# Kernel tuning notes

Hardware: AMD Instinct MI355X
Metric: run time of the kernel (lower is better)

Reference implementation:

```python
import jax, jax.numpy as jnp
import numpy as np

H = 128  # GRU hidden size


def gru_cell(x_t, h, W_ih, W_hh, b_ih, b_hh):
    # Standard torch GRU cell math.
    gi = x_t @ W_ih.T + b_ih            # (bs, 3H)
    gh = h @ W_hh.T + b_hh              # (bs, 3H)
    i_r, i_z, i_n = jnp.split(gi, 3, axis=-1)
    h_r, h_z, h_n = jnp.split(gh, 3, axis=-1)
    r = jax.nn.sigmoid(i_r + h_r)
    z = jax.nn.sigmoid(i_z + h_z)
    n = jnp.tanh(i_n + r * h_n)
    return (1.0 - z) * n + z * h


def setup_inputs() -> dict:
    key = jax.random.key(0)
    ks = jax.random.split(key, 16)
    bs, seq, emb, nc = 64, 1024, 300, 23
    s = 0.05
    inp = {
        "x": jax.random.normal(ks[0], (bs, seq, emb), jnp.float32),
        "adj": jax.random.uniform(ks[1], (bs, seq, seq), jnp.float32),
        "mask": jax.random.uniform(ks[2], (bs, seq, 1), jnp.float32),
        # GRU forward direction params (torch layout: W_ih (3H, emb), W_hh (3H, H))
        "W_ih_f": jax.random.normal(ks[3], (3 * H, emb), jnp.float32) * s,
        "W_hh_f": jax.random.normal(ks[4], (3 * H, H), jnp.float32) * s,
        "b_ih_f": jax.random.normal(ks[5], (3 * H,), jnp.float32) * s,
        "b_hh_f": jax.random.normal(ks[6], (3 * H,), jnp.float32) * s,
        # GRU backward direction params
        "W_ih_b": jax.random.normal(ks[7], (3 * H, emb), jnp.float32) * s,
        "W_hh_b": jax.random.normal(ks[8], (3 * H, H), jnp.float32) * s,
        "b_ih_b": jax.random.normal(ks[9], (3 * H,), jnp.float32) * s,
        "b_hh_b": jax.random.normal(ks[10], (3 * H,), jnp.float32) * s,
        # MLP head: Linear(300+256,128) -> Linear(128,64) -> Linear(64,23)
        "W1": jax.random.normal(ks[11], (128, emb + 2 * H), jnp.float32) * s,
        "b1": jnp.zeros((128,), jnp.float32),
        "W2": jax.random.normal(ks[12], (64, 128), jnp.float32) * s,
        "b2": jnp.zeros((64,), jnp.float32),
        "W3": jax.random.normal(ks[13], (nc, 64), jnp.float32) * s,
        "b3": jnp.zeros((nc,), jnp.float32),
    }
    return inp


def reference(x, adj, mask, W_ih_f, W_hh_f, b_ih_f, b_hh_f,
              W_ih_b, W_hh_b, b_ih_b, b_hh_b, W1, b1, W2, b2, W3, b3):
    x = x * mask                                   # (bs, seq, emb)
    bs, seq, emb = x.shape

    # --- bidirectional GRU, last-step output ---
    # Forward direction output at t = seq-1 is the final hidden of a full scan.
    h0 = jnp.zeros((bs, H), x.dtype)
    def step(h, x_t):
        h_new = gru_cell(x_t, h, W_ih_f, W_hh_f, b_ih_f, b_hh_f)
        return h_new, None
    h_fwd, _ = jax.lax.scan(step, h0, jnp.swapaxes(x, 0, 1))  # (bs, H)
    # Backward direction output at t = seq-1 is exactly ONE cell step on x[:, -1]
    # starting from the zero initial state (it has only consumed the last token).
    h_bwd = gru_cell(x[:, -1, :], h0, W_ih_b, W_hh_b, b_ih_b, b_hh_b)
    h = jnp.concatenate([h_fwd, h_bwd], axis=1)    # (bs, 2H)

    # --- gfm: sum_{i,j} x_i * x_j per feature == (sum_i x_i)^2 ---
    # (original code materializes a (bs, seq*seq, emb) tensor; adj is dead code)
    s = jnp.sum(x, axis=1)                         # (bs, emb)
    gfm = s * s                                    # (bs, emb)

    # --- MLP head (dropout is identity at eval) ---
    z = jnp.concatenate([h, gfm], axis=1)          # (bs, 2H + emb)
    z = jax.nn.relu(z @ W1.T + b1)
    z = jax.nn.relu(z @ W2.T + b2)
    logit = z @ W3.T + b3                          # (bs, num_class)
    return logit
```

## Files before the change

kernel.cpp:

```cpp
#include <hip/hip_runtime.h>
#include <hip/hip_bf16.h>

#define HH   128
#define EMB  300
#define SEQ  1024
#define BS   64
#define NG   384
#define NCHUNK 8

typedef __attribute__((ext_vector_type(8))) short  bf16x8;
typedef __attribute__((ext_vector_type(4))) float  f32x4;
typedef _Float16 f16x2 __attribute__((ext_vector_type(2)));

__device__ __forceinline__ unsigned short f2bf(float f) {
    unsigned int u = __float_as_uint(f);
    unsigned int r = (u + 0x7fffu + ((u >> 16) & 1u)) >> 16;
    return (unsigned short)r;
}
__device__ __forceinline__ float bf2f(unsigned short u) {
    return __uint_as_float((unsigned int)u << 16);
}
__device__ __forceinline__ float fexp(float x) { return __builtin_amdgcn_exp2f(x * 1.44269504088896f); }
__device__ __forceinline__ float fsig(float x) { return __builtin_amdgcn_rcpf(1.f + fexp(-x)); }
__device__ __forceinline__ float ftanh(float x){ return __builtin_amdgcn_rcpf(1.f + fexp(-2.f*x)) * 2.f - 1.f; }

__device__ __forceinline__ float dpp_pair_add(float x) {
    int y = __builtin_amdgcn_mov_dpp(__float_as_int(x), 0xB1, 0xF, 0xF, true);
    return x + __int_as_float(y);
}

#define BAR_LDS() asm volatile("s_waitcnt lgkmcnt(0)\n\ts_barrier" ::: "memory")

__global__ __launch_bounds__(512) void gi_gemm(const float* __restrict__ X,
                                               const float* __restrict__ mask,
                                               const float* __restrict__ W,
                                               const float* __restrict__ bias,
                                               const float* __restrict__ bhh2,
                                               unsigned short* __restrict__ out) {
    __shared__ __align__(16) unsigned short As[128 * 32];
    __shared__ __align__(16) unsigned short Bs[384 * 32];
    const int m0   = blockIdx.x * 128;
    const int tid  = threadIdx.x;
    const int row  = tid >> 2;
    const int seg  = tid & 3;
    const int wave = tid >> 6;
    const int lane = tid & 63;
    const int wm   = wave >> 2;
    const int wn   = wave & 3;
    const int r16  = lane & 15, kg = lane >> 4;

    f32x4 acc[4][6];
    #pragma unroll
    for (int m = 0; m < 4; ++m)
        #pragma unroll
        for (int n = 0; n < 6; ++n) acc[m][n] = (f32x4){0.f,0.f,0.f,0.f};

    const float mrow = mask[m0 + row];

    for (int k0 = 0; k0 < 320; k0 += 32) {
        {
            const float* src = X + (size_t)(m0 + row) * EMB + k0 + seg * 8;
            unsigned short tmp[8];
            if (k0 + seg * 8 + 7 < EMB) {
                float4 v0 = ((const float4*)src)[0];
                float4 v1 = ((const float4*)src)[1];
                tmp[0]=f2bf(v0.x*mrow); tmp[1]=f2bf(v0.y*mrow);
                tmp[2]=f2bf(v0.z*mrow); tmp[3]=f2bf(v0.w*mrow);
                tmp[4]=f2bf(v1.x*mrow); tmp[5]=f2bf(v1.y*mrow);
                tmp[6]=f2bf(v1.z*mrow); tmp[7]=f2bf(v1.w*mrow);
            } else {
                #pragma unroll
                for (int i = 0; i < 8; ++i) {
                    int c = k0 + seg * 8 + i;
                    float v = (c < EMB) ? src[i] : 0.f;
                    tmp[i] = f2bf(v * mrow);
                }
            }
            *(uint4*)&As[row * 32 + seg * 8] = *(const uint4*)tmp;
        }
        #pragma unroll
        for (int r3 = 0; r3 < 3; ++r3) {
            const int rowb = row + r3 * 128;
            const float* src = W + (size_t)rowb * EMB + k0 + seg * 8;
            unsigned short tmp[8];
            if (k0 + seg * 8 + 7 < EMB) {
                float4 v0 = ((const float4*)src)[0];
                float4 v1 = ((const float4*)src)[1];
                tmp[0]=f2bf(v0.x); tmp[1]=f2bf(v0.y); tmp[2]=f2bf(v0.z); tmp[3]=f2bf(v0.w);
                tmp[4]=f2bf(v1.x); tmp[5]=f2bf(v1.y); tmp[6]=f2bf(v1.z); tmp[7]=f2bf(v1.w);
            } else {
                #pragma unroll
                for (int i = 0; i < 8; ++i) {
                    int c = k0 + seg * 8 + i;
                    float v = (c < EMB) ? src[i] : 0.f;
                    tmp[i] = f2bf(v);
                }
            }
            *(uint4*)&Bs[rowb * 32 + seg * 8] = *(const uint4*)tmp;
        }
        __syncthreads();

        bf16x8 a[4], bfr[6];
        #pragma unroll
        for (int m = 0; m < 4; ++m)
            a[m] = *(const bf16x8*)&As[(wm * 64 + m * 16 + r16) * 32 + kg * 8];
        #pragma unroll
        for (int n = 0; n < 6; ++n)
            bfr[n] = *(const bf16x8*)&Bs[(wn * 96 + n * 16 + r16) * 32 + kg * 8];
        #pragma unroll
        for (int m = 0; m < 4; ++m)
            #pragma unroll
            for (int n = 0; n < 6; ++n)
                acc[m][n] = __builtin_amdgcn_mfma_f32_16x16x32_bf16(a[m], bfr[n], acc[m][n], 0, 0, 0);
        __syncthreads();
    }

    #pragma unroll
    for (int m = 0; m < 4; ++m) {
        const int rowb = m0 + wm * 64 + m * 16 + kg * 4;
        #pragma unroll
        for (int n = 0; n < 6; ++n) {
            const int col = wn * 96 + n * 16 + r16;
            const float bj = bias[col] + (col < 2 * HH ? bhh2[col] : 0.f);
            #pragma unroll
            for (int q = 0; q < 4; ++q)
                out[(size_t)(rowb + q) * NG + col] = f2bf(acc[m][n][q] + bj);
        }
    }
}

__global__ __launch_bounds__(320) void col_sum(const float* __restrict__ X,
                                               const float* __restrict__ mask,
                                               float* __restrict__ spart) {
    const int b = blockIdx.x, c = blockIdx.y;
    const int e = threadIdx.x;
    if (e >= EMB) return;
    const int tchunk = SEQ / NCHUNK;
    float acc = 0.f;
    const float* xb = X + ((size_t)b * SEQ + (size_t)c * tchunk) * EMB;
    const float* mb = mask + (size_t)b * SEQ + (size_t)c * tchunk;
    for (int t = 0; t < tchunk; ++t)
        acc += xb[(size_t)t * EMB + e] * mb[t];
    spart[((size_t)b * NCHUNK + c) * EMB + e] = acc;
}

__global__ __launch_bounds__(256, 1) void gru_scan(const unsigned short* __restrict__ gi,
                                                   const float* __restrict__ Whh,
                                                   const float* __restrict__ bhh,
                                                   float* __restrict__ hout) {
    const int b    = blockIdx.x;
    const int tid  = threadIdx.x;
    const int j    = tid >> 1;
    const int half = tid & 1;
    __shared__ __align__(16) _Float16 hb[2][HH];

    f16x2 wr_[32], wz_[32], wn_[32];
    {
        const float2* r0 = (const float2*)(Whh + (size_t)j * HH            + half * 64);
        const float2* r1 = (const float2*)(Whh + (size_t)(j + HH) * HH     + half * 64);
        const float2* r2 = (const float2*)(Whh + (size_t)(j + 2 * HH) * HH + half * 64);
        #pragma unroll
        for (int i = 0; i < 32; ++i) {
            float2 a = r0[i], c = r1[i], d = r2[i];
            wr_[i] = (f16x2){(_Float16)a.x, (_Float16)a.y};
            wz_[i] = (f16x2){(_Float16)c.x, (_Float16)c.y};
            wn_[i] = (f16x2){(_Float16)d.x, (_Float16)d.y};
        }
    }
    const float bn_ = bhh[j + 2 * HH];

    float hreg = 0.f;
    if (tid < HH) hb[0][tid] = (_Float16)0.f;
    const unsigned short* gb = gi + (size_t)b * SEQ * NG;

    float gAr, gAz, gAn, gBr, gBz, gBn, gCr, gCz, gCn, gDr, gDz, gDn;
    {
        const unsigned short* g0 = gb;          gAr = bf2f(g0[j]); gAz = bf2f(g0[j+HH]); gAn = bf2f(g0[j+2*HH]);
        const unsigned short* g1 = gb + NG;     gBr = bf2f(g1[j]); gBz = bf2f(g1[j+HH]); gBn = bf2f(g1[j+2*HH]);
        const unsigned short* g2 = gb + 2 * NG; gCr = bf2f(g2[j]); gCz = bf2f(g2[j+HH]); gCn = bf2f(g2[j+2*HH]);
        const unsigned short* g3 = gb + 3 * NG; gDr = bf2f(g3[j]); gDz = bf2f(g3[j+HH]); gDn = bf2f(g3[j+2*HH]);
    }
    const unsigned short* pA = gb + 4 * NG;
    const unsigned short* pB = gb + 5 * NG;
    const unsigned short* pC = gb + 6 * NG;
    const unsigned short* pD = gb + 7 * NG;
    BAR_LDS();

#define GRU_BODY(P, GR, GZ, GN, PP)                                            \
    {                                                                          \
        float ar[2] = {0.f, 0.f}, az[2] = {0.f, 0.f}, an[2] = {0.f, 0.f};      \
        const uint4* hp = (const uint4*)&hb[P][half * 64];                     \
        _Pragma("unroll")                                                      \
        for (int i = 0; i < 8; ++i) {                                          \
            union { uint4 u; f16x2 h2[4]; } U;                                 \
            U.u = hp[i];                                                       \
            _Pragma("unroll")                                                  \
            for (int k = 0; k < 4; ++k) {                                      \
                ar[k&1] = __builtin_amdgcn_fdot2(wr_[i*4+k], U.h2[k], ar[k&1], false); \
                az[k&1] = __builtin_amdgcn_fdot2(wz_[i*4+k], U.h2[k], az[k&1], false); \
                an[k&1] = __builtin_amdgcn_fdot2(wn_[i*4+k], U.h2[k], an[k&1], false); \
            }                                                                  \
        }                                                                      \
        const float arf = dpp_pair_add(ar[0] + ar[1]);                         \
        const float azf = dpp_pair_add(az[0] + az[1]);                         \
        const float anf = dpp_pair_add(an[0] + an[1]);                         \
        const float r = fsig(GR + arf);                                        \
        const float z = fsig(GZ + azf);                                        \
        const float n = ftanh(GN + r * (anf + bn_));                           \
        hreg = n + z * (hreg - n);                                             \
        if (!half) hb[P ^ 1][j] = (_Float16)hreg;                              \
        GR = bf2f(PP[j]); GZ = bf2f(PP[j + HH]); GN = bf2f(PP[j + 2 * HH]);    \
        PP += 4 * NG;                                                          \
        BAR_LDS();                                                             \
    }

    for (int it = 0; it < SEQ / 4; ++it) {
        GRU_BODY(0, gAr, gAz, gAn, pA)
        GRU_BODY(1, gBr, gBz, gBn, pB)
        GRU_BODY(0, gCr, gCz, gCn, pC)
        GRU_BODY(1, gDr, gDz, gDn, pD)
    }
#undef GRU_BODY
    if (!half) hout[b * HH + j] = hreg;
}

__global__ __launch_bounds__(128) void mlp(const float* __restrict__ X,
                                           const float* __restrict__ mask,
                                           const float* __restrict__ WihB,
                                           const float* __restrict__ bihB,
                                           const float* __restrict__ bhhB,
                                           const float* __restrict__ hf,
                                           const float* __restrict__ spart,
                                           const float* __restrict__ W1, const float* __restrict__ b1,
                                           const float* __restrict__ W2, const float* __restrict__ b2,
                                           const float* __restrict__ W3, const float* __restrict__ b3,
                                           float* __restrict__ out) {
    const int b = blockIdx.x, j = threadIdx.x;
    __shared__ float xl[EMB];
    __shared__ float zin[2 * HH + EMB];
    __shared__ float l1[128];
    __shared__ float l2[64];

    const float* xr = X + ((size_t)b * SEQ + (SEQ - 1)) * EMB;
    const float  mv = mask[(size_t)b * SEQ + SEQ - 1];
    for (int e = j; e < EMB; e += 128) xl[e] = xr[e];
    zin[j] = hf[b * HH + j];
    for (int e = j; e < EMB; e += 128) {
        float v = 0.f;
        #pragma unroll
        for (int c = 0; c < NCHUNK; ++c)
            v += spart[((size_t)b * NCHUNK + c) * EMB + e];
        zin[2 * HH + e] = v * v;
    }
    __syncthreads();

    {
        const float* wR = WihB + (size_t)j * EMB;
        const float* wZ = WihB + (size_t)(j + HH) * EMB;
        const float* wN = WihB + (size_t)(j + 2 * HH) * EMB;
        float aR = 0.f, aZ = 0.f, aN = 0.f;
        for (int e = 0; e < EMB; ++e) {
            const float xv = xl[e];
            aR += xv * wR[e]; aZ += xv * wZ[e]; aN += xv * wN[e];
        }
        const float r = fsig(aR * mv + bihB[j] + bhhB[j]);
        const float z = fsig(aZ * mv + bihB[j + HH] + bhhB[j + HH]);
        const float n = ftanh(aN * mv + bihB[j + 2 * HH] + r * bhhB[j + 2 * HH]);
        zin[HH + j] = (1.f - z) * n;
    }
    __syncthreads();

    {
        float a = b1[j];
        const float* w = W1 + (size_t)j * (2 * HH + EMB);
        for (int i = 0; i < 2 * HH + EMB; ++i) a += zin[i] * w[i];
        l1[j] = fmaxf(a, 0.f);
    }
    __syncthreads();
    if (j < 64) {
        float a = b2[j];
        const float* w = W2 + (size_t)j * 128;
        for (int i = 0; i < 128; ++i) a += l1[i] * w[i];
        l2[j] = fmaxf(a, 0.f);
    }
    __syncthreads();
    if (j < 23) {
        float a = b3[j];
        const float* w = W3 + (size_t)j * 64;
        for (int i = 0; i < 64; ++i) a += l2[i] * w[i];
        out[b * 23 + j] = a;
    }
}

extern "C" void kernel_launch(void* const* d_in, const int* in_sizes, int n_in,
                              void* d_out, int out_size, void* d_ws, size_t ws_size,
                              hipStream_t stream) {
    const float* x     = (const float*)d_in[0];
    const float* mask  = (const float*)d_in[2];
    const float* Wih_f = (const float*)d_in[3];
    const float* Whh_f = (const float*)d_in[4];
    const float* bih_f = (const float*)d_in[5];
    const float* bhh_f = (const float*)d_in[6];
    const float* Wih_b = (const float*)d_in[7];
    const float* bih_b = (const float*)d_in[9];
    const float* bhh_b = (const float*)d_in[10];
    const float* W1 = (const float*)d_in[11];
    const float* b1 = (const float*)d_in[12];
    const float* W2 = (const float*)d_in[13];
    const float* b2 = (const float*)d_in[14];
    const float* W3 = (const float*)d_in[15];
    const float* b3 = (const float*)d_in[16];
    float* out = (float*)d_out;

    unsigned short* gi16 = (unsigned short*)d_ws;
    float* spart = (float*)(gi16 + (size_t)BS * SEQ * NG);
    float* hf    = spart + (size_t)BS * NCHUNK * EMB;

    gi_gemm<<<dim3(512), dim3(512), 0, stream>>>(x, mask, Wih_f, bih_f, bhh_f, gi16);
    col_sum<<<dim3(BS, NCHUNK), dim3(320), 0, stream>>>(x, mask, spart);
    gru_scan<<<dim3(BS), dim3(256), 0, stream>>>(gi16, Whh_f, bhh_f, hf);
    mlp<<<dim3(BS), dim3(128), 0, stream>>>(x, mask, Wih_b, bih_b, bhh_b, hf, spart,
                                            W1, b1, W2, b2, W3, b3, out);
}
```

Measured before the change: 579.0 us.

## Batch GRU recurrence across 16 sequences per block using f16 MFMA

The recurrent h@W_hh product moves from per-sequence fdot2 with one block per batch element to 16x16x32 f16 MFMA instructions, batching 16 sequences per block. That cuts the grid to 4 blocks, with weights held in registers as MFMA fragments and hidden state exchanged through a swizzled LDS buffer. The input-gate buffer also goes from bf16 to fp32, doubling its memory traffic but removing conversions and bf16 rounding error. The risk is that only 4 CUs are used for the sequential scan, and each step now loads more gi data per thread.

```diff
diff --git a/kernel.cpp b/kernel.cpp
--- a/kernel.cpp
+++ b/kernel.cpp
@@ -10,24 +10,16 @@
 
 typedef __attribute__((ext_vector_type(8))) short  bf16x8;
 typedef __attribute__((ext_vector_type(4))) float  f32x4;
-typedef _Float16 f16x2 __attribute__((ext_vector_type(2)));
+typedef _Float16 f16x8 __attribute__((ext_vector_type(8)));
 
 __device__ __forceinline__ unsigned short f2bf(float f) {
     unsigned int u = __float_as_uint(f);
     unsigned int r = (u + 0x7fffu + ((u >> 16) & 1u)) >> 16;
     return (unsigned short)r;
 }
-__device__ __forceinline__ float bf2f(unsigned short u) {
-    return __uint_as_float((unsigned int)u << 16);
-}
 __device__ __forceinline__ float fexp(float x) { return __builtin_amdgcn_exp2f(x * 1.44269504088896f); }
 __device__ __forceinline__ float fsig(float x) { return __builtin_amdgcn_rcpf(1.f + fexp(-x)); }
 __device__ __forceinline__ float ftanh(float x){ return __builtin_amdgcn_rcpf(1.f + fexp(-2.f*x)) * 2.f - 1.f; }
-
-__device__ __forceinline__ float dpp_pair_add(float x) {
-    int y = __builtin_amdgcn_mov_dpp(__float_as_int(x), 0xB1, 0xF, 0xF, true);
-    return x + __int_as_float(y);
-}
 
 #define BAR_LDS() asm volatile("s_waitcnt lgkmcnt(0)\n\ts_barrier" ::: "memory")
 
@@ -36,7 +28,7 @@
                                                const float* __restrict__ W,
                                                const float* __restrict__ bias,
                                                const float* __restrict__ bhh2,
-                                               unsigned short* __restrict__ out) {
+                                               float* __restrict__ out) {
     __shared__ __align__(16) unsigned short As[128 * 32];
     __shared__ __align__(16) unsigned short Bs[384 * 32];
     const int m0   = blockIdx.x * 128;
@@ -124,7 +116,7 @@
             const float bj = bias[col] + (col < 2 * HH ? bhh2[col] : 0.f);
             #pragma unroll
             for (int q = 0; q < 4; ++q)
-                out[(size_t)(rowb + q) * NG + col] = f2bf(acc[m][n][q] + bj);
+                out[(size_t)(rowb + q) * NG + col] = acc[m][n][q] + bj;
         }
     }
 }
@@ -144,84 +136,117 @@
     spart[((size_t)b * NCHUNK + c) * EMB + e] = acc;
 }
 
-__global__ __launch_bounds__(256, 1) void gru_scan(const unsigned short* __restrict__ gi,
+__global__ __launch_bounds__(256, 1) void gru_scan(const float* __restrict__ gi,
                                                    const float* __restrict__ Whh,
                                                    const float* __restrict__ bhh,
                                                    float* __restrict__ hout) {
-    const int b    = blockIdx.x;
     const int tid  = threadIdx.x;
-    const int j    = tid >> 1;
-    const int half = tid & 1;
-    __shared__ __align__(16) _Float16 hb[2][HH];
-
-    f16x2 wr_[32], wz_[32], wn_[32];
-    {
-        const float2* r0 = (const float2*)(Whh + (size_t)j * HH            + half * 64);
-        const float2* r1 = (const float2*)(Whh + (size_t)(j + HH) * HH     + half * 64);
-        const float2* r2 = (const float2*)(Whh + (size_t)(j + 2 * HH) * HH + half * 64);
-        #pragma unroll
-        for (int i = 0; i < 32; ++i) {
-            float2 a = r0[i], c = r1[i], d = r2[i];
-            wr_[i] = (f16x2){(_Float16)a.x, (_Float16)a.y};
-            wz_[i] = (f16x2){(_Float16)c.x, (_Float16)c.y};
-            wn_[i] = (f16x2){(_Float16)d.x, (_Float16)d.y};
-        }
-    }
-    const float bn_ = bhh[j + 2 * HH];
-
-    float hreg = 0.f;
-    if (tid < HH) hb[0][tid] = (_Float16)0.f;
-    const unsigned short* gb = gi + (size_t)b * SEQ * NG;
-
-    float gAr, gAz, gAn, gBr, gBz, gBn, gCr, gCz, gCn, gDr, gDz, gDn;
-    {
-        const unsigned short* g0 = gb;          gAr = bf2f(g0[j]); gAz = bf2f(g0[j+HH]); gAn = bf2f(g0[j+2*HH]);
-        const unsigned short* g1 = gb + NG;     gBr = bf2f(g1[j]); gBz = bf2f(g1[j+HH]); gBn = bf2f(g1[j+2*HH]);
-        const unsigned short* g2 = gb + 2 * NG; gCr = bf2f(g2[j]); gCz = bf2f(g2[j+HH]); gCn = bf2f(g2[j+2*HH]);
-        const unsigned short* g3 = gb + 3 * NG; gDr = bf2f(g3[j]); gDz = bf2f(g3[j+HH]); gDn = bf2f(g3[j+2*HH]);
-    }
-    const unsigned short* pA = gb + 4 * NG;
-    const unsigned short* pB = gb + 5 * NG;
-    const unsigned short* pC = gb + 6 * NG;
-    const unsigned short* pD = gb + 7 * NG;
+    const int w    = tid >> 6;
+    const int lane = tid & 63;
+    const int r16  = lane & 15;
+    const int kg   = lane >> 4;
+    const int bg   = blockIdx.x * 16 + r16;
+    const int jA   = w * 32 + kg * 4;
+    const int jB   = jA + 16;
+
+    __shared__ _Float16 hl[2][16][16][8];
+
+    f16x8 wf[2][3][4];
+    #pragma unroll
+    for (int g = 0; g < 2; ++g)
+        #pragma unroll
+        for (int gt = 0; gt < 3; ++gt)
+            #pragma unroll
+            for (int ks = 0; ks < 4; ++ks) {
+                const float* src = Whh + (size_t)(gt * HH + w * 32 + g * 16 + r16) * HH + ks * 32 + kg * 8;
+                float4 v0 = *(const float4*)src;
+                float4 v1 = *(const float4*)(src + 4);
+                wf[g][gt][ks] = (f16x8){(_Float16)v0.x,(_Float16)v0.y,(_Float16)v0.z,(_Float16)v0.w,
+                                        (_Float16)v1.x,(_Float16)v1.y,(_Float16)v1.z,(_Float16)v1.w};
+            }
+    const f32x4 bnA_ = *(const f32x4*)&bhh[2 * HH + jA];
+    const f32x4 bnB_ = *(const f32x4*)&bhh[2 * HH + jB];
+
+    for (int i = tid; i < 2 * 16 * 16 * 8 / 2; i += 256) ((unsigned int*)hl)[i] = 0;
+    f32x4 hA = (f32x4){0.f,0.f,0.f,0.f};
+    f32x4 hB = (f32x4){0.f,0.f,0.f,0.f};
+
+    const float* gbase = gi + (size_t)bg * SEQ * NG;
+    const float* p0 = gbase;
+    const float* p1 = gbase + NG;
+    f32x4 G0rA = *(const f32x4*)(p0 + jA);
+    f32x4 G0rB = *(const f32x4*)(p0 + jB);
+    f32x4 G0zA = *(const f32x4*)(p0 + HH + jA);
+    f32x4 G0zB = *(const f32x4*)(p0 + HH + jB);
+    f32x4 G0nA = *(const f32x4*)(p0 + 2 * HH + jA);
+    f32x4 G0nB = *(const f32x4*)(p0 + 2 * HH + jB);
+    f32x4 G1rA = *(const f32x4*)(p1 + jA);
+    f32x4 G1rB = *(const f32x4*)(p1 + jB);
+    f32x4 G1zA = *(const f32x4*)(p1 + HH + jA);
+    f32x4 G1zB = *(const f32x4*)(p1 + HH + jB);
+    f32x4 G1nA = *(const f32x4*)(p1 + 2 * HH + jA);
+    f32x4 G1nB = *(const f32x4*)(p1 + 2 * HH + jB);
+    p0 += 2 * NG; p1 += 2 * NG;
+    const int cA = 4 * w + (kg >> 1);
+    const int cB = cA + 2;
+    const int oW = (kg & 1) * 4;
     BAR_LDS();
 
-#define GRU_BODY(P, GR, GZ, GN, PP)                                            \
+#define GRU_BODY(P, GrA, GrB, GzA, GzB, GnA, GnB, PP)                          \
     {                                                                          \
-        float ar[2] = {0.f, 0.f}, az[2] = {0.f, 0.f}, an[2] = {0.f, 0.f};      \
-        const uint4* hp = (const uint4*)&hb[P][half * 64];                     \
+        f16x8 hbf[4];                                                          \
         _Pragma("unroll")                                                      \
-        for (int i = 0; i < 8; ++i) {                                          \
-            union { uint4 u; f16x2 h2[4]; } U;                                 \
-            U.u = hp[i];                                                       \
-            _Pragma("unroll")                                                  \
-            for (int k = 0; k < 4; ++k) {                                      \
-                ar[k&1] = __builtin_amdgcn_fdot2(wr_[i*4+k], U.h2[k], ar[k&1], false); \
-                az[k&1] = __builtin_amdgcn_fdot2(wz_[i*4+k], U.h2[k], az[k&1], false); \
-                an[k&1] = __builtin_amdgcn_fdot2(wn_[i*4+k], U.h2[k], an[k&1], false); \
-            }                                                                  \
+        for (int ks = 0; ks < 4; ++ks) {                                       \
+            const int c = ks * 4 + kg;                                         \
+            hbf[ks] = *(const f16x8*)&hl[P][c][(r16 + c) & 15][0];             \
         }                                                                      \
-        const float arf = dpp_pair_add(ar[0] + ar[1]);                         \
-        const float azf = dpp_pair_add(az[0] + az[1]);                         \
-        const float anf = dpp_pair_add(an[0] + an[1]);                         \
-        const float r = fsig(GR + arf);                                        \
-        const float z = fsig(GZ + azf);                                        \
-        const float n = ftanh(GN + r * (anf + bn_));                           \
-        hreg = n + z * (hreg - n);                                             \
-        if (!half) hb[P ^ 1][j] = (_Float16)hreg;                              \
-        GR = bf2f(PP[j]); GZ = bf2f(PP[j + HH]); GN = bf2f(PP[j + 2 * HH]);    \
-        PP += 4 * NG;                                                          \
+        f32x4 aRA=(f32x4){0.f,0.f,0.f,0.f}, aRB=(f32x4){0.f,0.f,0.f,0.f};     \
+        f32x4 aZA=(f32x4){0.f,0.f,0.f,0.f}, aZB=(f32x4){0.f,0.f,0.f,0.f};     \
+        f32x4 aNA=(f32x4){0.f,0.f,0.f,0.f}, aNB=(f32x4){0.f,0.f,0.f,0.f};     \
+        _Pragma("unroll")                                                      \
+        for (int ks = 0; ks < 4; ++ks) {                                       \
+            const f16x8 hb = hbf[ks];                                          \
+            aRA = __builtin_amdgcn_mfma_f32_16x16x32_f16(wf[0][0][ks], hb, aRA, 0, 0, 0); \
+            aRB = __builtin_amdgcn_mfma_f32_16x16x32_f16(wf[1][0][ks], hb, aRB, 0, 0, 0); \
+            aZA = __builtin_amdgcn_mfma_f32_16x16x32_f16(wf[0][1][ks], hb, aZA, 0, 0, 0); \
+            aZB = __builtin_amdgcn_mfma_f32_16x16x32_f16(wf[1][1][ks], hb, aZB, 0, 0, 0); \
+            aNA = __builtin_amdgcn_mfma_f32_16x16x32_f16(wf[0][2][ks], hb, aNA, 0, 0, 0); \
+            aNB = __builtin_amdgcn_mfma_f32_16x16x32_f16(wf[1][2][ks], hb, aNB, 0, 0, 0); \
+        }                                                                      \
+        union { _Float16 h4[4]; uint2 u; } WA, WB;                             \
+        _Pragma("unroll")                                                      \
+        for (int q = 0; q < 4; ++q) {                                          \
+            const float rA = fsig(GrA[q] + aRA[q]);                            \
+            const float zA = fsig(GzA[q] + aZA[q]);                            \
+            const float nA = ftanh(GnA[q] + rA * (aNA[q] + bnA_[q]));          \
+            hA[q] = nA + zA * (hA[q] - nA);                                    \
+            WA.h4[q] = (_Float16)hA[q];                                        \
+            const float rB = fsig(GrB[q] + aRB[q]);                            \
+            const float zB = fsig(GzB[q] + aZB[q]);                            \
+            const float nB = ftanh(GnB[q] + rB * (aNB[q] + bnB_[q]));          \
+            hB[q] = nB + zB * (hB[q] - nB);                                    \
+            WB.h4[q] = (_Float16)hB[q];                                        \
+        }                                                                      \
+        *(uint2*)&hl[P ^ 1][cA][(r16 + cA) & 15][oW] = WA.u;                   \
+        *(uint2*)&hl[P ^ 1][cB][(r16 + cB) & 15][oW] = WB.u;                   \
+        GrA = *(const f32x4*)(PP + jA);                                        \
+        GrB = *(const f32x4*)(PP + jB);                                        \
+        GzA = *(const f32x4*)(PP + HH + jA);                                   \
+        GzB = *(const f32x4*)(PP + HH + jB);                                   \
+        GnA = *(const f32x4*)(PP + 2 * HH + jA);                               \
+        GnB = *(const f32x4*)(PP + 2 * HH + jB);                               \
+        PP += 2 * NG;                                                          \
         BAR_LDS();                                                             \
     }
 
-    for (int it = 0; it < SEQ / 4; ++it) {
-        GRU_BODY(0, gAr, gAz, gAn, pA)
-        GRU_BODY(1, gBr, gBz, gBn, pB)
-        GRU_BODY(0, gCr, gCz, gCn, pC)
-        GRU_BODY(1, gDr, gDz, gDn, pD)
+    for (int it = 0; it < SEQ / 2; ++it) {
+        GRU_BODY(0, G0rA, G0rB, G0zA, G0zB, G0nA, G0nB, p0)
+        GRU_BODY(1, G1rA, G1rB, G1zA, G1zB, G1nA, G1nB, p1)
     }
 #undef GRU_BODY
-    if (!half) hout[b * HH + j] = hreg;
+
+    *(float4*)&hout[(size_t)bg * HH + jA] = (float4){hA[0], hA[1], hA[2], hA[3]};
+    *(float4*)&hout[(size_t)bg * HH + jB] = (float4){hB[0], hB[1], hB[2], hB[3]};
 }
 
 __global__ __launch_bounds__(128) void mlp(const float* __restrict__ X,
@@ -312,13 +337,13 @@
     const float* b3 = (const float*)d_in[16];
     float* out = (float*)d_out;
 
-    unsigned short* gi16 = (unsigned short*)d_ws;
-    float* spart = (float*)(gi16 + (size_t)BS * SEQ * NG);
+    float* gi    = (float*)d_ws;
+    float* spart = gi + (size_t)BS * SEQ * NG;
     float* hf    = spart + (size_t)BS * NCHUNK * EMB;
 
-    gi_gemm<<<dim3(512), dim3(512), 0, stream>>>(x, mask, Wih_f, bih_f, bhh_f, gi16);
+    gi_gemm<<<dim3(512), dim3(512), 0, stream>>>(x, mask, Wih_f, bih_f, bhh_f, gi);
     col_sum<<<dim3(BS, NCHUNK), dim3(320), 0, stream>>>(x, mask, spart);
-    gru_scan<<<dim3(BS), dim3(256), 0, stream>>>(gi16, Whh_f, bhh_f, hf);
+    gru_scan<<<dim3(4), dim3(256), 0, stream>>>(gi, Whh_f, bhh_f, hf);
     mlp<<<dim3(BS), dim3(128), 0, stream>>>(x, mask, Wih_b, bih_b, bhh_b, hf, spart,
                                             W1, b1, W2, b2, W3, b3, out);
 }
```

New measurement: 892.9 us. +54.2%, slower.

## Store gate inputs as fp32 and use packed fp16 FMA accumulation in GRU scan

Applied to the files above, without the earlier changes.

The input-projection GEMM now writes fp32 gate inputs instead of bf16, so the scan loads floats directly without conversion. The recurrent matvec now accumulates in packed half2 FMAs with fp16 accumulators instead of fdot2 with fp32 accumulators, then reduces to fp32. This aims to shorten the serial per-step latency of the recurrence. In exchange, the gi intermediate doubles in memory traffic, and fp16 accumulation over 1024 steps may lose accuracy.

```diff
diff --git a/kernel.cpp b/kernel.cpp
--- a/kernel.cpp
+++ b/kernel.cpp
@@ -17,9 +17,6 @@
     unsigned int r = (u + 0x7fffu + ((u >> 16) & 1u)) >> 16;
     return (unsigned short)r;
 }
-__device__ __forceinline__ float bf2f(unsigned short u) {
-    return __uint_as_float((unsigned int)u << 16);
-}
 __device__ __forceinline__ float fexp(float x) { return __builtin_amdgcn_exp2f(x * 1.44269504088896f); }
 __device__ __forceinline__ float fsig(float x) { return __builtin_amdgcn_rcpf(1.f + fexp(-x)); }
 __device__ __forceinline__ float ftanh(float x){ return __builtin_amdgcn_rcpf(1.f + fexp(-2.f*x)) * 2.f - 1.f; }
@@ -36,7 +33,7 @@
                                                const float* __restrict__ W,
                                                const float* __restrict__ bias,
                                                const float* __restrict__ bhh2,
-                                               unsigned short* __restrict__ out) {
+                                               float* __restrict__ out) {
     __shared__ __align__(16) unsigned short As[128 * 32];
     __shared__ __align__(16) unsigned short Bs[384 * 32];
     const int m0   = blockIdx.x * 128;
@@ -124,7 +121,7 @@
             const float bj = bias[col] + (col < 2 * HH ? bhh2[col] : 0.f);
             #pragma unroll
             for (int q = 0; q < 4; ++q)
-                out[(size_t)(rowb + q) * NG + col] = f2bf(acc[m][n][q] + bj);
+                out[(size_t)(rowb + q) * NG + col] = acc[m][n][q] + bj;
         }
     }
 }
@@ -144,7 +141,7 @@
     spart[((size_t)b * NCHUNK + c) * EMB + e] = acc;
 }
 
-__global__ __launch_bounds__(256, 1) void gru_scan(const unsigned short* __restrict__ gi,
+__global__ __launch_bounds__(256, 1) void gru_scan(const float* __restrict__ gi,
                                                    const float* __restrict__ Whh,
                                                    const float* __restrict__ bhh,
                                                    float* __restrict__ hout) {
@@ -171,45 +168,58 @@
 
     float hreg = 0.f;
     if (tid < HH) hb[0][tid] = (_Float16)0.f;
-    const unsigned short* gb = gi + (size_t)b * SEQ * NG;
+    const float* gb = gi + (size_t)b * SEQ * NG;
 
     float gAr, gAz, gAn, gBr, gBz, gBn, gCr, gCz, gCn, gDr, gDz, gDn;
     {
-        const unsigned short* g0 = gb;          gAr = bf2f(g0[j]); gAz = bf2f(g0[j+HH]); gAn = bf2f(g0[j+2*HH]);
-        const unsigned short* g1 = gb + NG;     gBr = bf2f(g1[j]); gBz = bf2f(g1[j+HH]); gBn = bf2f(g1[j+2*HH]);
-        const unsigned short* g2 = gb + 2 * NG; gCr = bf2f(g2[j]); gCz = bf2f(g2[j+HH]); gCn = bf2f(g2[j+2*HH]);
-        const unsigned short* g3 = gb + 3 * NG; gDr = bf2f(g3[j]); gDz = bf2f(g3[j+HH]); gDn = bf2f(g3[j+2*HH]);
-    }
-    const unsigned short* pA = gb + 4 * NG;
-    const unsigned short* pB = gb + 5 * NG;
-    const unsigned short* pC = gb + 6 * NG;
-    const unsigned short* pD = gb + 7 * NG;
+        const float* g0 = gb;               gAr = g0[j]; gAz = g0[j+HH]; gAn = g0[j+2*HH];
+        const float* g1 = gb + NG;          gBr = g1[j]; gBz = g1[j+HH]; gBn = g1[j+2*HH];
+        const float* g2 = gb + 2 * NG;      gCr = g2[j]; gCz = g2[j+HH]; gCn = g2[j+2*HH];
+        const float* g3 = gb + 3 * NG;      gDr = g3[j]; gDz = g3[j+HH]; gDn = g3[j+2*HH];
+    }
+    const float* pA = gb + 4 * NG;
+    const float* pB = gb + 5 * NG;
+    const float* pC = gb + 6 * NG;
+    const float* pD = gb + 7 * NG;
     BAR_LDS();
+
+    const f16x2 Z2 = (f16x2){(_Float16)0.f, (_Float16)0.f};
 
 #define GRU_BODY(P, GR, GZ, GN, PP)                                            \
     {                                                                          \
-        float ar[2] = {0.f, 0.f}, az[2] = {0.f, 0.f}, an[2] = {0.f, 0.f};      \
+        f16x2 ar0=Z2, ar1=Z2, ar2=Z2, ar3=Z2;                                  \
+        f16x2 az0=Z2, az1=Z2, az2=Z2, az3=Z2;                                  \
+        f16x2 an0=Z2, an1=Z2, an2=Z2, an3=Z2;                                  \
         const uint4* hp = (const uint4*)&hb[P][half * 64];                     \
         _Pragma("unroll")                                                      \
         for (int i = 0; i < 8; ++i) {                                          \
             union { uint4 u; f16x2 h2[4]; } U;                                 \
             U.u = hp[i];                                                       \
-            _Pragma("unroll")                                                  \
-            for (int k = 0; k < 4; ++k) {                                      \
-                ar[k&1] = __builtin_amdgcn_fdot2(wr_[i*4+k], U.h2[k], ar[k&1], false); \
-                az[k&1] = __builtin_amdgcn_fdot2(wz_[i*4+k], U.h2[k], az[k&1], false); \
-                an[k&1] = __builtin_amdgcn_fdot2(wn_[i*4+k], U.h2[k], an[k&1], false); \
-            }                                                                  \
+            ar0 = wr_[i*4+0] * U.h2[0] + ar0;                                  \
+            ar1 = wr_[i*4+1] * U.h2[1] + ar1;                                  \
+            ar2 = wr_[i*4+2] * U.h2[2] + ar2;                                  \
+            ar3 = wr_[i*4+3] * U.h2[3] + ar3;                                  \
+            az0 = wz_[i*4+0] * U.h2[0] + az0;                                  \
+            az1 = wz_[i*4+1] * U.h2[1] + az1;                                  \
+            az2 = wz_[i*4+2] * U.h2[2] + az2;                                  \
+            az3 = wz_[i*4+3] * U.h2[3] + az3;                                  \
+            an0 = wn_[i*4+0] * U.h2[0] + an0;                                  \
+            an1 = wn_[i*4+1] * U.h2[1] + an1;                                  \
+            an2 = wn_[i*4+2] * U.h2[2] + an2;                                  \
+            an3 = wn_[i*4+3] * U.h2[3] + an3;                                  \
         }                                                                      \
-        const float arf = dpp_pair_add(ar[0] + ar[1]);                         \
-        const float azf = dpp_pair_add(az[0] + az[1]);                         \
-        const float anf = dpp_pair_add(an[0] + an[1]);                         \
+        f16x2 sr = (ar0 + ar1) + (ar2 + ar3);                                  \
+        f16x2 sz = (az0 + az1) + (az2 + az3);                                  \
+        f16x2 sn = (an0 + an1) + (an2 + an3);                                  \
+        const float arf = dpp_pair_add((float)sr[0] + (float)sr[1]);           \
+        const float azf = dpp_pair_add((float)sz[0] + (float)sz[1]);           \
+        const float anf = dpp_pair_add((float)sn[0] + (float)sn[1]);           \
         const float r = fsig(GR + arf);                                        \
         const float z = fsig(GZ + azf);                                        \
         const float n = ftanh(GN + r * (anf + bn_));                           \
         hreg = n + z * (hreg - n);                                             \
         if (!half) hb[P ^ 1][j] = (_Float16)hreg;                              \
-        GR = bf2f(PP[j]); GZ = bf2f(PP[j + HH]); GN = bf2f(PP[j + 2 * HH]);    \
+        GR = PP[j]; GZ = PP[j + HH]; GN = PP[j + 2 * HH];                      \
         PP += 4 * NG;                                                          \
         BAR_LDS();                                                             \
     }
@@ -312,13 +322,13 @@
     const float* b3 = (const float*)d_in[16];
     float* out = (float*)d_out;
 
-    unsigned short* gi16 = (unsigned short*)d_ws;
-    float* spart = (float*)(gi16 + (size_t)BS * SEQ * NG);
+    float* gi    = (float*)d_ws;
+    float* spart = gi + (size_t)BS * SEQ * NG;
     float* hf    = spart + (size_t)BS * NCHUNK * EMB;
 
-    gi_gemm<<<dim3(512), dim3(512), 0, stream>>>(x, mask, Wih_f, bih_f, bhh_f, gi16);
+    gi_gemm<<<dim3(512), dim3(512), 0, stream>>>(x, mask, Wih_f, bih_f, bhh_f, gi);
     col_sum<<<dim3(BS, NCHUNK), dim3(320), 0, stream>>>(x, mask, spart);
-    gru_scan<<<dim3(BS), dim3(256), 0, stream>>>(gi16, Whh_f, bhh_f, hf);
+    gru_scan<<<dim3(BS), dim3(256), 0, stream>>>(gi, Whh_f, bhh_f, hf);
     mlp<<<dim3(BS), dim3(128), 0, stream>>>(x, mask, Wih_b, bih_b, bhh_b, hf, spart,
                                             W1, b1, W2, b2, W3, b3, out);
 }
```

New measurement: 577.6 us. Within noise of the previous version (-0.2%).
